# Kernel tuning notes

Hardware: AMD Instinct MI355X
Metric: run time of the kernel (lower is better)

## Reference

```python
import jax, jax.numpy as jnp
import numpy as np

N, E, T, S, R, L = 100000, 1600000, 4, 32, 16, 5
H = 3 * S  # out-head hidden (hidden_list=[n_scalars*3])
EPS = 1e-8


def _mlp(x, W1, b1, W2, b2):
    return jax.nn.silu(x @ W1 + b1) @ W2 + b2


def setup_inputs() -> dict:
    key = jax.random.key(0)
    ks = iter(jax.random.split(key, 40))
    rn = lambda *s: jax.random.normal(next(ks), s, dtype=jnp.float32)
    p = lambda *s: rn(*s) * 0.1
    inp = {
        'u': rn(N, T),
        'v': rn(N, T, 2),
        'boundary_norm': rn(N, 2),
        'is_boundary': jnp.zeros((N,), dtype=bool),
        'y_force': rn(N, 2),
        'pos': rn(N, 2),
        'edge_index': jax.random.randint(next(ks), (2, E), 0, N, dtype=jnp.int64),
        # node embedding MLP: invariant feats (2T+2) -> 2S -> S
        'Wn1': p(2 * T + 2, 2 * S), 'bn1': jnp.zeros((2 * S,)),
        'Wn2': p(2 * S, S), 'bn2': jnp.zeros((S,)),
        # L stacked InvBlock params: edge MLP (2S+R -> S -> S), node update (2S -> S -> S)
        'We1': p(L, 2 * S + R, S), 'be1': jnp.zeros((L, S)),
        'We2': p(L, S, S), 'be2': jnp.zeros((L, S)),
        'Wu1': p(L, 2 * S, S), 'bu1': jnp.zeros((L, S)),
        'Wu2': p(L, S, S), 'bu2': jnp.zeros((L, S)),
        'ln_g': jnp.ones((S,)), 'ln_b': jnp.zeros((S,)),
        # heads: S -> 3S -> {2,1}
        'Wr1': p(S, H), 'br1': jnp.zeros((H,)), 'Wr2': p(H, 2), 'br2': jnp.zeros((2,)),
        'Ws1': p(S, H), 'bs1': jnp.zeros((H,)), 'Ws2': p(H, 1), 'bs2': jnp.zeros((1,)),
    }
    return inp


def _forward(u, v, boundary_norm, y_force, pos, edge_index,
             Wn1, bn1, Wn2, bn2, We1, be1, We2, be2, Wu1, bu1, Wu2, bu2,
             ln_g, ln_b, Wr1, br1, Wr2, br2, Ws1, bs1, Ws2, bs2):
    # torch.no_grad() geometry branch: center positions, edge distances
    posc = jax.lax.stop_gradient(pos - pos.mean(axis=0))
    row, col = edge_index[0], edge_index[1]
    edge_vec = posc[row] - posc[col]                       # [E,2]
    dist = jnp.linalg.norm(edge_vec, axis=1)               # [E]
    # besel_linspace(start=0, end=1, number=R, cutoff=False): Bessel/sine RBF
    freqs = jnp.arange(1, R + 1, dtype=jnp.float32) * jnp.pi
    rbf = jnp.sqrt(2.0) * jnp.sin(dist[:, None] * freqs) / (dist[:, None] + EPS)  # [E,R]

    # Node_embedding_inv: SE(2)-invariant scalar features -> MLP
    feats = jnp.concatenate([
        u,                                                 # [N,T]
        jnp.linalg.norm(v, axis=-1),                       # [N,T]
        jnp.linalg.norm(boundary_norm, axis=-1, keepdims=True),
        jnp.linalg.norm(y_force, axis=-1, keepdims=True),
    ], axis=-1)                                            # [N,2T+2]
    x = _mlp(feats, Wn1, bn1, Wn2, bn2)                    # [N,S]

    # degree for mean aggregation (computed once)
    deg = jax.ops.segment_sum(jnp.ones((E,), jnp.float32), row, num_segments=N)
    inv_deg = 1.0 / jnp.maximum(deg, 1.0)                  # [N]

    for l in range(L):  # InvBlock message passing
        ef = jnp.concatenate([x[row], x[col], rbf], axis=-1)   # [E,2S+R]
        m = _mlp(ef, We1[l], be1[l], We2[l], be2[l])           # [E,S]
        agg = jax.ops.segment_sum(m, row, num_segments=N) * inv_deg[:, None]
        x = x + _mlp(jnp.concatenate([x, agg], axis=-1), Wu1[l], bu1[l], Wu2[l], bu2[l])

    # LayerNorm
    mu = x.mean(axis=-1, keepdims=True)
    var = jnp.var(x, axis=-1, keepdims=True)
    x = (x - mu) * jax.lax.rsqrt(var + 1e-5) * ln_g + ln_b

    v_ = _mlp(x, Wr1, br1, Wr2, br2)                       # [N,2]
    u_ = _mlp(x, Ws1, bs1, Ws2, bs2)                       # [N,1]
    return u[:, -1] + u_[:, 0], v_ + v[:, -1, :]


def reference(u, v, boundary_norm, is_boundary, y_force, pos, edge_index,
              Wn1, bn1, Wn2, bn2, We1, be1, We2, be2, Wu1, bu1, Wu2, bu2,
              ln_g, ln_b, Wr1, br1, Wr2, br2, Ws1, bs1, Ws2, bs2):
    del is_boundary  # unused by the visible forward
    return _forward(u, v, boundary_norm, y_force, pos, edge_index,
                    Wn1, bn1, Wn2, bn2, We1, be1, We2, be2, Wu1, bu1, Wu2, bu2,
                    ln_g, ln_b, Wr1, br1, Wr2, br2, Ws1, bs1, Ws2, bs2)
```

## Files before the change

### kernel.cpp

```cpp
#include <hip/hip_runtime.h>
#include <cmath>

namespace {

constexpr int N = 100000;
constexpr int E = 1600000;
constexpr int S = 32;
constexpr int L = 5;
constexpr int NB = (N + 255) / 256;
constexpr int NPW = 16;
constexpr int LB2 = (N + 63) / 64;
constexpr int NBKT = 391;
constexpr int EPB  = E / 256;
constexpr float PI_F    = 3.14159265358979323846f;
constexpr float SQRT2_F = 1.41421356237309515f;

typedef __attribute__((ext_vector_type(8))) short short8;
typedef __attribute__((ext_vector_type(4))) float f32x4;

__device__ __forceinline__ float silu_f(float x) {
    return x * __builtin_amdgcn_rcpf(1.0f + __expf(-x));
}

__device__ __forceinline__ unsigned short f2bf(float f) {
    unsigned int u = __float_as_uint(f);
    u = (u + 0x7FFFu + ((u >> 16) & 1u)) >> 16;
    return (unsigned short)u;
}

__device__ __forceinline__ int rl(int v, int i) {
    return __builtin_amdgcn_readlane(v, i);
}

__device__ __forceinline__ short8 ld_xb(const unsigned short* base, int col, int quad) {
    unsigned off = ((unsigned)col << 6) | ((unsigned)quad << 4);
    return *reinterpret_cast<const short8*>(reinterpret_cast<const char*>(base) + off);
}

__device__ __forceinline__ short8 ld_rbf(const unsigned short* base, int slot, int quad) {
    unsigned off = ((unsigned)slot << 5) | ((unsigned)quad << 4);
    return *reinterpret_cast<const short8*>(reinterpret_cast<const char*>(base) + off);
}

__device__ __forceinline__ void adv(int& i, int& t, int vd) {
    ++t;
    while (i < 16) {
        int dgi = rl(vd, i);
        int nt = (dgi + 15) >> 4;
        if (t < nt) break;
        t = 0; ++i;
    }
}

__device__ __forceinline__ int slotOf(int i, int t, int vs, int vd, int ml) {
    if (i >= 16) return 0;
    int s0 = rl(vs, i);
    int dg = rl(vd, i);
    int smax = s0 + ((dg > 0) ? dg : 1) - 1;
    int s = s0 + t * 16 + ml;
    return min(s, smax);
}

__global__ __launch_bounds__(256) void passA_kernel(
    const int* __restrict__ ei, int* __restrict__ hist)
{
    __shared__ int h[NBKT];
    int t = threadIdx.x;
    int blk = blockIdx.x;
    for (int b = t; b < NBKT; b += 256) h[b] = 0;
    __syncthreads();
    int base = blk * EPB;
    for (int i = t; i < EPB; i += 256) {
        int r = ei[base + i];
        atomicAdd(&h[r >> 8], 1);
    }
    __syncthreads();
    for (int b = t; b < NBKT; b += 256) hist[b * 256 + blk] = h[b];
}

__global__ __launch_bounds__(512) void p1_kernel(
    const int* __restrict__ hist, int* __restrict__ bstart)
{
    __shared__ int tot[NBKT + 1];
    int t = threadIdx.x;
    if (t < NBKT) {
        int s = 0;
        for (int b = 0; b < 256; ++b) s += hist[t * 256 + b];
        tot[t] = s;
    }
    __syncthreads();
    if (t == 0) {
        int a = 0;
        for (int i = 0; i < NBKT; ++i) { int c = tot[i]; tot[i] = a; a += c; }
        tot[NBKT] = a;
    }
    __syncthreads();
    if (t <= NBKT) bstart[t] = tot[t];
}

__global__ __launch_bounds__(256) void p2_kernel(
    const int* __restrict__ hist, const int* __restrict__ bstart,
    int* __restrict__ base)
{
    __shared__ int pre[256];
    int t = threadIdx.x;
    int bin = blockIdx.x;
    int h = hist[bin * 256 + t];
    pre[t] = h;
    __syncthreads();
    #pragma unroll
    for (int off = 1; off < 256; off <<= 1) {
        int v = (t >= off) ? pre[t - off] : 0;
        __syncthreads();
        pre[t] += v;
        __syncthreads();
    }
    base[bin * 256 + t] = bstart[bin] + pre[t] - h;
}

__global__ __launch_bounds__(256) void passB_kernel(
    const int* __restrict__ ei, const float* __restrict__ pos,
    const int* __restrict__ base, uint4* __restrict__ edgebuf)
{
    __shared__ int cur[NBKT];
    int t = threadIdx.x;
    int blk = blockIdx.x;
    for (int b = t; b < NBKT; b += 256) cur[b] = base[b * 256 + blk];
    __syncthreads();
    int ebase = blk * EPB;
    for (int i = t; i < EPB; i += 256) {
        int e = ebase + i;
        int r = ei[e];
        int c = ei[E + e];
        float2 pr = reinterpret_cast<const float2*>(pos)[r];
        float2 pc = reinterpret_cast<const float2*>(pos)[c];
        float dx = pr.x - pc.x, dy = pr.y - pc.y;
        float d = sqrtf(dx * dx + dy * dy);
        int slot = atomicAdd(&cur[r >> 8], 1);
        edgebuf[slot] = make_uint4((unsigned)c, __float_as_uint(d), (unsigned)r, 0u);
    }
}

__global__ __launch_bounds__(256) void passC_kernel(
    const uint4* __restrict__ edgebuf, const int* __restrict__ bstart,
    int* __restrict__ deg, int* __restrict__ start,
    int* __restrict__ csr_col, unsigned short* __restrict__ rbf_buf)
{
    __shared__ int cnt[256];
    __shared__ int pre[256];
    __shared__ int cur[256];
    int t = threadIdx.x;
    int bkt = blockIdx.x;
    int s0 = bstart[bkt], s1 = bstart[bkt + 1];

    cnt[t] = 0;
    __syncthreads();
    for (int i = s0 + t; i < s1; i += 256) {
        unsigned r = edgebuf[i].z;
        atomicAdd(&cnt[r & 255], 1);
    }
    __syncthreads();
    int c0 = cnt[t];
    pre[t] = c0;
    __syncthreads();
    #pragma unroll
    for (int off = 1; off < 256; off <<= 1) {
        int v = (t >= off) ? pre[t - off] : 0;
        __syncthreads();
        pre[t] += v;
        __syncthreads();
    }
    int row = bkt * 256 + t;
    int st = s0 + pre[t] - c0;
    if (row < N) {
        deg[row] = c0;
        start[row] = st;
    }
    cur[t] = st;
    __syncthreads();

    for (int i = s0 + t; i < s1; i += 256) {
        uint4 e = edgebuf[i];
        int slot = atomicAdd(&cur[e.z & 255], 1);
        csr_col[slot] = (int)e.x;
        float d = __uint_as_float(e.y);

        float sn = __sinf(PI_F * d);
        float c1 = __cosf(PI_F * d);
        float inv = SQRT2_F / (d + 1e-8f);
        float tc = 2.0f * c1;
        float sk = sn, skm = 0.0f;
        unsigned int pk[8];
        #pragma unroll
        for (int k = 0; k < 8; ++k) {
            float r0 = sk * inv;
            float s2 = tc * sk - skm; skm = sk; sk = s2;
            float r1 = sk * inv;
            float s3 = tc * sk - skm; skm = sk; sk = s3;
            pk[k] = (unsigned int)f2bf(r0) | ((unsigned int)f2bf(r1) << 16);
        }
        uint4* out = reinterpret_cast<uint4*>(rbf_buf + (size_t)slot * 16);
        out[0] = make_uint4(pk[0], pk[1], pk[2], pk[3]);
        out[1] = make_uint4(pk[4], pk[5], pk[6], pk[7]);
    }
}

__global__ __launch_bounds__(256) void prep_wt_kernel(
    const float* __restrict__ We1, const float* __restrict__ We2,
    const float* __restrict__ Wu1, const float* __restrict__ Wu2,
    short* __restrict__ wt1, short* __restrict__ wt2,
    short* __restrict__ wtu1, short* __restrict__ wtu2)
{
    int idx = blockIdx.x * 256 + threadIdx.x;
    if (idx < 5 * 32 * 96) {
        int l = idx / (32 * 96), r = idx % (32 * 96), n = r / 96, k = r % 96;
        float v = (k < 80) ? We1[((size_t)l * 80 + k) * 32 + n] : 0.0f;
        wt1[idx] = (short)f2bf(v);
    }
    if (idx < 5 * 32 * 32) {
        int l = idx / 1024, r = idx % 1024, n = r / 32, k = r % 32;
        wt2[idx]  = (short)f2bf(We2[((size_t)l * 32 + k) * 32 + n]);
        wtu2[idx] = (short)f2bf(Wu2[((size_t)l * 32 + k) * 32 + n]);
    }
    if (idx < 5 * 32 * 64) {
        int l = idx / 2048, r = idx % 2048, n = r / 64, k = r % 64;
        wtu1[idx] = (short)f2bf(Wu1[((size_t)l * 64 + k) * 32 + n]);
    }
}

__global__ __launch_bounds__(256) void node_embed_kernel(
    const float* __restrict__ u, const float* __restrict__ v,
    const float* __restrict__ bnorm, const float* __restrict__ yf,
    const float* __restrict__ Wn1, const float* __restrict__ bn1,
    const float* __restrict__ Wn2, const float* __restrict__ bn2,
    float* __restrict__ x, unsigned short* __restrict__ xb)
{
    int n = blockIdx.x * 256 + threadIdx.x;
    if (n >= N) return;

    float f[10];
    float4 uu = reinterpret_cast<const float4*>(u)[n];
    f[0] = uu.x; f[1] = uu.y; f[2] = uu.z; f[3] = uu.w;
    float4 v0 = reinterpret_cast<const float4*>(v)[2 * n];
    float4 v1 = reinterpret_cast<const float4*>(v)[2 * n + 1];
    f[4] = sqrtf(v0.x * v0.x + v0.y * v0.y);
    f[5] = sqrtf(v0.z * v0.z + v0.w * v0.w);
    f[6] = sqrtf(v1.x * v1.x + v1.y * v1.y);
    f[7] = sqrtf(v1.z * v1.z + v1.w * v1.w);
    float2 bb = reinterpret_cast<const float2*>(bnorm)[n];
    f[8] = sqrtf(bb.x * bb.x + bb.y * bb.y);
    float2 yy = reinterpret_cast<const float2*>(yf)[n];
    f[9] = sqrtf(yy.x * yy.x + yy.y * yy.y);

    float h[64];
    #pragma unroll
    for (int j = 0; j < 64; ++j) h[j] = bn1[j];
    #pragma unroll
    for (int i = 0; i < 10; ++i) {
        float t = f[i];
        #pragma unroll
        for (int j = 0; j < 64; ++j) h[j] = fmaf(t, Wn1[i * 64 + j], h[j]);
    }
    #pragma unroll
    for (int j = 0; j < 64; ++j) h[j] = silu_f(h[j]);

    float o[32];
    #pragma unroll
    for (int j = 0; j < 32; ++j) o[j] = bn2[j];
    #pragma unroll
    for (int i = 0; i < 64; ++i) {
        float t = h[i];
        #pragma unroll
        for (int j = 0; j < 32; ++j) o[j] = fmaf(t, Wn2[i * 32 + j], o[j]);
    }
    float4* xo = reinterpret_cast<float4*>(x + (size_t)n * 32);
    #pragma unroll
    for (int i = 0; i < 8; ++i)
        xo[i] = make_float4(o[4 * i], o[4 * i + 1], o[4 * i + 2], o[4 * i + 3]);

    unsigned int* xbu = reinterpret_cast<unsigned int*>(xb) + (size_t)n * 16;
    #pragma unroll
    for (int i = 0; i < 16; ++i)
        xbu[i] = (unsigned int)f2bf(o[2 * i]) | ((unsigned int)f2bf(o[2 * i + 1]) << 16);
}

__global__ __launch_bounds__(256, 4) void layer_kernel(
    const int* __restrict__ deg, const int* __restrict__ start,
    const int* __restrict__ csr_col, const unsigned short* __restrict__ rbf_buf,
    const float* __restrict__ x_in, const unsigned short* __restrict__ xb_in,
    float* __restrict__ x_out, unsigned short* __restrict__ xb_out,
    const short* __restrict__ wt1, const float* __restrict__ b1,
    const short* __restrict__ wt2, const float* __restrict__ b2,
    const short* __restrict__ wtu1, const float* __restrict__ bu1,
    const short* __restrict__ wtu2, const float* __restrict__ bu2)
{
    __shared__ unsigned short lsh[4][16 * 34];
    __shared__ unsigned short agb[4][16 * 34];
    __shared__ unsigned short hub[4][16 * 34];
    __shared__ float lx[4][16 * 33];
    __shared__ float lrp[4][16 * 33];
    __shared__ float ldg[4][16];
    __shared__ float livd[4][16];

    int t = threadIdx.x;
    int w = t >> 6;
    int lane = t & 63;
    int quad = lane >> 4;
    int ml = lane & 15;
    int wid = blockIdx.x * 4 + w;
    int nbase = __builtin_amdgcn_readfirstlane(wid * NPW);
    if (nbase >= N) return;

    int vs = start[nbase + ml];
    int vd = deg[nbase + ml];

    const short8* wp = reinterpret_cast<const short8*>(wt1);
    short8 B00 = wp[(ml     ) * 12 + 0 * 4 + quad];
    short8 B01 = wp[(ml     ) * 12 + 1 * 4 + quad];
    short8 B02 = wp[(ml     ) * 12 + 2 * 4 + quad];
    short8 B10 = wp[(ml + 16) * 12 + 0 * 4 + quad];
    short8 B11 = wp[(ml + 16) * 12 + 1 * 4 + quad];
    short8 B12 = wp[(ml + 16) * 12 + 2 * 4 + quad];

    short8 Ax = ld_xb(xb_in, nbase + ml, quad);

    float b1j0 = b1[ml];
    float b1j1 = b1[ml + 16];

    unsigned short* lshp = lsh[w];
    for (int k = lane; k < 16 * 34; k += 64) lshp[k] = 0;
    {
        const float* xs = x_in + (size_t)nbase * 32;
        float* lxp = lx[w];
        #pragma unroll
        for (int k = 0; k < 8; ++k) {
            int idx = lane * 8 + k;
            lxp[(idx >> 5) * 33 + (idx & 31)] = xs[idx];
        }
    }
    if (lane < 16) {
        ldg[w][lane] = (float)vd;
        livd[w][lane] = 1.0f / fmaxf((float)vd, 1.0f);
    }

    float* rpp = lrp[w];
    {
        f32x4 rp0 = {b1j0, b1j0, b1j0, b1j0};
        f32x4 rp1 = {b1j1, b1j1, b1j1, b1j1};
        rp0 = __builtin_amdgcn_mfma_f32_16x16x32_bf16(Ax, B00, rp0, 0, 0, 0);
        rp1 = __builtin_amdgcn_mfma_f32_16x16x32_bf16(Ax, B10, rp1, 0, 0, 0);
        int row = quad * 4;
        #pragma unroll
        for (int r = 0; r < 4; ++r) {
            rpp[(row + r) * 33 + ml]      = rp0[r];
            rpp[(row + r) * 33 + ml + 16] = rp1[r];
        }
    }
    __builtin_amdgcn_wave_barrier();

    const short8 Z8 = {0, 0, 0, 0, 0, 0, 0, 0};
    int i0 = 0, t0 = -1; adv(i0, t0, vd);
    int i1 = i0, t1 = t0; adv(i1, t1, vd);
    int i2 = i1, t2 = t1; adv(i2, t2, vd);

    int slot0 = slotOf(i0, t0, vs, vd, ml);
    int slot1 = slotOf(i1, t1, vs, vd, ml);
    int colCur  = csr_col[slot0];
    int colNext = csr_col[slot1];
    short8 A1c = ld_xb(xb_in, colCur, quad);
    short8 A2c = Z8;
    if (quad < 2) A2c = ld_rbf(rbf_buf, slot0, quad);

    float colp0 = 0.0f, colp1 = 0.0f;
    while (i0 < 16) {
        int slot2 = slotOf(i2, t2, vs, vd, ml);
        int colNN = csr_col[slot2];
        short8 A1n = ld_xb(xb_in, colNext, quad);
        short8 A2n = Z8;
        if (quad < 2) A2n = ld_rbf(rbf_buf, slot1, quad);

        float rpa = rpp[i0 * 33 + ml];
        float rpb = rpp[i0 * 33 + ml + 16];
        f32x4 acc0 = {rpa, rpa, rpa, rpa};
        f32x4 acc1 = {rpb, rpb, rpb, rpb};
        acc0 = __builtin_amdgcn_mfma_f32_16x16x32_bf16(A1c, B01, acc0, 0, 0, 0);
        acc0 = __builtin_amdgcn_mfma_f32_16x16x32_bf16(A2c, B02, acc0, 0, 0, 0);
        acc1 = __builtin_amdgcn_mfma_f32_16x16x32_bf16(A1c, B11, acc1, 0, 0, 0);
        acc1 = __builtin_amdgcn_mfma_f32_16x16x32_bf16(A2c, B12, acc1, 0, 0, 0);

        int dg0 = rl(vd, i0);
        int rowbase = t0 * 16 + quad * 4;
        #pragma unroll
        for (int r = 0; r < 4; ++r) {
            bool vld = (rowbase + r) < dg0;
            colp0 += vld ? silu_f(acc0[r]) : 0.0f;
            colp1 += vld ? silu_f(acc1[r]) : 0.0f;
        }
        if (t0 == ((dg0 + 15) >> 4) - 1) {
            colp0 += __shfl_xor(colp0, 16, 64);
            colp0 += __shfl_xor(colp0, 32, 64);
            colp1 += __shfl_xor(colp1, 16, 64);
            colp1 += __shfl_xor(colp1, 32, 64);
            if (quad == 0) {
                lshp[i0 * 34 + ml]      = f2bf(colp0);
                lshp[i0 * 34 + ml + 16] = f2bf(colp1);
            }
            colp0 = 0.0f; colp1 = 0.0f;
        }

        A1c = A1n; A2c = A2n;
        colNext = colNN; slot1 = slot2;
        i0 = i1; t0 = t1; i1 = i2; t1 = t2;
        adv(i2, t2, vd);
    }
    __builtin_amdgcn_wave_barrier();

    const short8* w2p = reinterpret_cast<const short8*>(wt2);
    short8 Bw2_0 = w2p[(ml     ) * 4 + quad];
    short8 Bw2_1 = w2p[(ml + 16) * 4 + quad];
    const short8* u1p = reinterpret_cast<const short8*>(wtu1);
    short8 Bu1_00 = u1p[(ml     ) * 8 + quad];
    short8 Bu1_10 = u1p[(ml     ) * 8 + 4 + quad];
    short8 Bu1_01 = u1p[(ml + 16) * 8 + quad];
    short8 Bu1_11 = u1p[(ml + 16) * 8 + 4 + quad];
    const short8* u2p = reinterpret_cast<const short8*>(wtu2);
    short8 Bu2_0 = u2p[(ml     ) * 4 + quad];
    short8 Bu2_1 = u2p[(ml + 16) * 4 + quad];

    short8 Ash = *reinterpret_cast<const short8*>(lshp + ml * 34 + quad * 8);
    f32x4 c0 = {0.0f, 0.0f, 0.0f, 0.0f};
    f32x4 c1 = {0.0f, 0.0f, 0.0f, 0.0f};
    c0 = __builtin_amdgcn_mfma_f32_16x16x32_bf16(Ash, Bw2_0, c0, 0, 0, 0);
    c1 = __builtin_amdgcn_mfma_f32_16x16x32_bf16(Ash, Bw2_1, c1, 0, 0, 0);
    float b2c0 = b2[ml], b2c1 = b2[ml + 16];
    unsigned short* agp = agb[w];
    int row = quad * 4;
    #pragma unroll
    for (int r = 0; r < 4; ++r) {
        float fd = ldg[w][row + r];
        float iv = livd[w][row + r];
        agp[(row + r) * 34 + ml]      = f2bf((c0[r] + fd * b2c0) * iv);
        agp[(row + r) * 34 + ml + 16] = f2bf((c1[r] + fd * b2c1) * iv);
    }
    __builtin_amdgcn_wave_barrier();

    short8 Aag = *reinterpret_cast<const short8*>(agp + ml * 34 + quad * 8);
    f32x4 d0 = {0.0f, 0.0f, 0.0f, 0.0f};
    f32x4 d1 = {0.0f, 0.0f, 0.0f, 0.0f};
    d0 = __builtin_amdgcn_mfma_f32_16x16x32_bf16(Ax,  Bu1_00, d0, 0, 0, 0);
    d0 = __builtin_amdgcn_mfma_f32_16x16x32_bf16(Aag, Bu1_10, d0, 0, 0, 0);
    d1 = __builtin_amdgcn_mfma_f32_16x16x32_bf16(Ax,  Bu1_01, d1, 0, 0, 0);
    d1 = __builtin_amdgcn_mfma_f32_16x16x32_bf16(Aag, Bu1_11, d1, 0, 0, 0);
    float bu1c0 = bu1[ml], bu1c1 = bu1[ml + 16];
    unsigned short* hup = hub[w];
    #pragma unroll
    for (int r = 0; r < 4; ++r) {
        hup[(row + r) * 34 + ml]      = f2bf(silu_f(d0[r] + bu1c0));
        hup[(row + r) * 34 + ml + 16] = f2bf(silu_f(d1[r] + bu1c1));
    }
    __builtin_amdgcn_wave_barrier();

    short8 Ahu = *reinterpret_cast<const short8*>(hup + ml * 34 + quad * 8);
    f32x4 e0 = {0.0f, 0.0f, 0.0f, 0.0f};
    f32x4 e1 = {0.0f, 0.0f, 0.0f, 0.0f};
    e0 = __builtin_amdgcn_mfma_f32_16x16x32_bf16(Ahu, Bu2_0, e0, 0, 0, 0);
    e1 = __builtin_amdgcn_mfma_f32_16x16x32_bf16(Ahu, Bu2_1, e1, 0, 0, 0);
    float bu2c0 = bu2[ml], bu2c1 = bu2[ml + 16];
    #pragma unroll
    for (int r = 0; r < 4; ++r) {
        int nn = nbase + row + r;
        float o0 = e0[r] + bu2c0 + lx[w][(row + r) * 33 + ml];
        float o1 = e1[r] + bu2c1 + lx[w][(row + r) * 33 + ml + 16];
        x_out[(size_t)nn * 32 + ml]      = o0;
        x_out[(size_t)nn * 32 + ml + 16] = o1;
        xb_out[(size_t)nn * 32 + ml]      = f2bf(o0);
        xb_out[(size_t)nn * 32 + ml + 16] = f2bf(o1);
    }
}

__global__ __launch_bounds__(256) void final_kernel(
    const float* __restrict__ x, const float* __restrict__ u,
    const float* __restrict__ v,
    const float* __restrict__ ln_g, const float* __restrict__ ln_b,
    const float* __restrict__ Wr1, const float* __restrict__ br1,
    const float* __restrict__ Wr2, const float* __restrict__ br2,
    const float* __restrict__ Ws1, const float* __restrict__ bs1,
    const float* __restrict__ Ws2, const float* __restrict__ bs2,
    float* __restrict__ out)
{
    int n = blockIdx.x * 256 + threadIdx.x;
    if (n >= N) return;

    float a[32];
    const float4* x4 = reinterpret_cast<const float4*>(x + (size_t)n * 32);
    #pragma unroll
    for (int i = 0; i < 8; ++i) {
        float4 t = x4[i];
        a[4 * i] = t.x; a[4 * i + 1] = t.y; a[4 * i + 2] = t.z; a[4 * i + 3] = t.w;
    }
    float mu = 0.0f;
    #pragma unroll
    for (int i = 0; i < 32; ++i) mu += a[i];
    mu *= (1.0f / 32.0f);
    float var = 0.0f;
    #pragma unroll
    for (int i = 0; i < 32; ++i) { float dlt = a[i] - mu; var += dlt * dlt; }
    var *= (1.0f / 32.0f);
    float rs = rsqrtf(var + 1e-5f);
    #pragma unroll
    for (int i = 0; i < 32; ++i) a[i] = (a[i] - mu) * rs * ln_g[i] + ln_b[i];

    float o0 = br2[0], o1 = br2[1], o2 = bs2[0];
    #pragma unroll 1
    for (int j = 0; j < 96; ++j) {
        float hr = br1[j];
        float hs = bs1[j];
        #pragma unroll
        for (int i = 0; i < 32; ++i) {
            hr = fmaf(a[i], Wr1[i * 96 + j], hr);
            hs = fmaf(a[i], Ws1[i * 96 + j], hs);
        }
        hr = silu_f(hr);
        hs = silu_f(hs);
        o0 = fmaf(hr, Wr2[2 * j], o0);
        o1 = fmaf(hr, Wr2[2 * j + 1], o1);
        o2 = fmaf(hs, Ws2[j], o2);
    }
    out[n] = u[n * 4 + 3] + o2;
    out[N + 2 * n]     = o0 + v[n * 8 + 6];
    out[N + 2 * n + 1] = o1 + v[n * 8 + 7];
}

}

extern "C" void kernel_launch(void* const* d_in, const int* in_sizes, int n_in,
                              void* d_out, int out_size, void* d_ws, size_t ws_size,
                              hipStream_t stream)
{
    const float* u    = (const float*)d_in[0];
    const float* v    = (const float*)d_in[1];
    const float* bno  = (const float*)d_in[2];
    const float* yf   = (const float*)d_in[4];
    const float* pos  = (const float*)d_in[5];
    const int*   ei   = (const int*)d_in[6];
    const float* Wn1  = (const float*)d_in[7];
    const float* bn1  = (const float*)d_in[8];
    const float* Wn2  = (const float*)d_in[9];
    const float* bn2  = (const float*)d_in[10];
    const float* We1  = (const float*)d_in[11];
    const float* be1  = (const float*)d_in[12];
    const float* We2  = (const float*)d_in[13];
    const float* be2  = (const float*)d_in[14];
    const float* Wu1  = (const float*)d_in[15];
    const float* bu1  = (const float*)d_in[16];
    const float* Wu2  = (const float*)d_in[17];
    const float* bu2  = (const float*)d_in[18];
    const float* ln_g = (const float*)d_in[19];
    const float* ln_b = (const float*)d_in[20];
    const float* Wr1  = (const float*)d_in[21];
    const float* br1  = (const float*)d_in[22];
    const float* Wr2  = (const float*)d_in[23];
    const float* br2  = (const float*)d_in[24];
    const float* Ws1  = (const float*)d_in[25];
    const float* bs1  = (const float*)d_in[26];
    const float* Ws2  = (const float*)d_in[27];
    const float* bs2  = (const float*)d_in[28];
    float* out = (float*)d_out;

    int*   deg      = (int*)d_ws;
    int*   start    = deg + N;
    int*   bstart   = start + N;
    int*   csr_col  = bstart + 512;
    unsigned short* rbf = (unsigned short*)(csr_col + E);
    float* x0       = (float*)(rbf + (size_t)E * 16);
    float* x1       = x0 + (size_t)N * S;
    unsigned short* xb0 = (unsigned short*)(x1 + (size_t)N * S);
    unsigned short* xb1 = xb0 + (size_t)N * S;
    short* wt1      = (short*)(xb1 + (size_t)N * S);
    short* wt2      = wt1 + 5 * 32 * 96;
    short* wtu1     = wt2 + 5 * 32 * 32;
    short* wtu2     = wtu1 + 5 * 32 * 64;
    int*   hist     = (int*)(wtu2 + 5 * 32 * 32);
    int*   basem    = hist + NBKT * 256;

    uint4* edgebuf = (uint4*)x0;

    passA_kernel<<<256, 256, 0, stream>>>(ei, hist);
    p1_kernel<<<1, 512, 0, stream>>>(hist, bstart);
    p2_kernel<<<NBKT, 256, 0, stream>>>(hist, bstart, basem);
    passB_kernel<<<256, 256, 0, stream>>>(ei, pos, basem, edgebuf);
    passC_kernel<<<NBKT, 256, 0, stream>>>(edgebuf, bstart, deg, start, csr_col, rbf);
    prep_wt_kernel<<<60, 256, 0, stream>>>(We1, We2, Wu1, Wu2, wt1, wt2, wtu1, wtu2);

    node_embed_kernel<<<NB, 256, 0, stream>>>(u, v, bno, yf, Wn1, bn1, Wn2, bn2,
                                              x0, xb0);

    float* xin = x0;  float* xout = x1;
    unsigned short* xbin = xb0;  unsigned short* xbout = xb1;
    for (int l = 0; l < L; ++l) {
        layer_kernel<<<LB2, 256, 0, stream>>>(
            deg, start, csr_col, rbf, xin, xbin, xout, xbout,
            wt1 + (size_t)l * 32 * 96,  be1 + (size_t)l * 32,
            wt2 + (size_t)l * 32 * 32,  be2 + (size_t)l * 32,
            wtu1 + (size_t)l * 32 * 64, bu1 + (size_t)l * 32,
            wtu2 + (size_t)l * 32 * 32, bu2 + (size_t)l * 32);
        float* tf = xin; xin = xout; xout = tf;
        unsigned short* tb = xbin; xbin = xbout; xbout = tb;
    }

    final_kernel<<<NB, 256, 0, stream>>>(xin, u, v, ln_g, ln_b,
                                         Wr1, br1, Wr2, br2,
                                         Ws1, bs1, Ws2, bs2, out);
}
```

Measured before the change: 572.6 us.

## Move output-head MLPs in final kernel onto bf16 MFMA

```diff
diff --git a/kernel.cpp b/kernel.cpp
--- a/kernel.cpp
+++ b/kernel.cpp
@@ -208,8 +208,10 @@
 __global__ __launch_bounds__(256) void prep_wt_kernel(
     const float* __restrict__ We1, const float* __restrict__ We2,
     const float* __restrict__ Wu1, const float* __restrict__ Wu2,
+    const float* __restrict__ Wr1, const float* __restrict__ Ws1,
     short* __restrict__ wt1, short* __restrict__ wt2,
-    short* __restrict__ wtu1, short* __restrict__ wtu2)
+    short* __restrict__ wtu1, short* __restrict__ wtu2,
+    short* __restrict__ wtr1, short* __restrict__ wts1)
 {
     int idx = blockIdx.x * 256 + threadIdx.x;
     if (idx < 5 * 32 * 96) {
@@ -225,6 +227,11 @@
     if (idx < 5 * 32 * 64) {
         int l = idx / 2048, r = idx % 2048, n = r / 64, k = r % 64;
         wtu1[idx] = (short)f2bf(Wu1[((size_t)l * 64 + k) * 32 + n]);
+    }
+    if (idx < 96 * 32) {
+        int n = idx / 32, k = idx % 32;
+        wtr1[idx] = (short)f2bf(Wr1[k * 96 + n]);
+        wts1[idx] = (short)f2bf(Ws1[k * 96 + n]);
     }
 }
 
@@ -482,53 +489,97 @@
     const float* __restrict__ x, const float* __restrict__ u,
     const float* __restrict__ v,
     const float* __restrict__ ln_g, const float* __restrict__ ln_b,
-    const float* __restrict__ Wr1, const float* __restrict__ br1,
+    const short* __restrict__ wtr1, const float* __restrict__ br1,
     const float* __restrict__ Wr2, const float* __restrict__ br2,
-    const float* __restrict__ Ws1, const float* __restrict__ bs1,
+    const short* __restrict__ wts1, const float* __restrict__ bs1,
     const float* __restrict__ Ws2, const float* __restrict__ bs2,
     float* __restrict__ out)
 {
-    int n = blockIdx.x * 256 + threadIdx.x;
-    if (n >= N) return;
-
-    float a[32];
-    const float4* x4 = reinterpret_cast<const float4*>(x + (size_t)n * 32);
-    #pragma unroll
-    for (int i = 0; i < 8; ++i) {
-        float4 t = x4[i];
-        a[4 * i] = t.x; a[4 * i + 1] = t.y; a[4 * i + 2] = t.z; a[4 * i + 3] = t.w;
-    }
-    float mu = 0.0f;
-    #pragma unroll
-    for (int i = 0; i < 32; ++i) mu += a[i];
-    mu *= (1.0f / 32.0f);
-    float var = 0.0f;
-    #pragma unroll
-    for (int i = 0; i < 32; ++i) { float dlt = a[i] - mu; var += dlt * dlt; }
-    var *= (1.0f / 32.0f);
+    int t = threadIdx.x;
+    int w = t >> 6;
+    int lane = t & 63;
+    int quad = lane >> 4;
+    int ml = lane & 15;
+    int wid = blockIdx.x * 4 + w;
+    int nbase = __builtin_amdgcn_readfirstlane(wid * NPW);
+    if (nbase >= N) return;
+
+    const float4* xs = reinterpret_cast<const float4*>(
+        x + (size_t)(nbase + ml) * 32 + quad * 8);
+    float4 xa = xs[0], xb4 = xs[1];
+    float f[8] = {xa.x, xa.y, xa.z, xa.w, xb4.x, xb4.y, xb4.z, xb4.w};
+
+    float s = 0.0f, ss = 0.0f;
+    #pragma unroll
+    for (int i = 0; i < 8; ++i) { s += f[i]; ss += f[i] * f[i]; }
+    s  += __shfl_xor(s, 16, 64);  s  += __shfl_xor(s, 32, 64);
+    ss += __shfl_xor(ss, 16, 64); ss += __shfl_xor(ss, 32, 64);
+    float mu = s * (1.0f / 32.0f);
+    float var = ss * (1.0f / 32.0f) - mu * mu;
     float rs = rsqrtf(var + 1e-5f);
-    #pragma unroll
-    for (int i = 0; i < 32; ++i) a[i] = (a[i] - mu) * rs * ln_g[i] + ln_b[i];
-
-    float o0 = br2[0], o1 = br2[1], o2 = bs2[0];
-    #pragma unroll 1
-    for (int j = 0; j < 96; ++j) {
-        float hr = br1[j];
-        float hs = bs1[j];
-        #pragma unroll
-        for (int i = 0; i < 32; ++i) {
-            hr = fmaf(a[i], Wr1[i * 96 + j], hr);
-            hs = fmaf(a[i], Ws1[i * 96 + j], hs);
+
+    const float4* gp = reinterpret_cast<const float4*>(ln_g + quad * 8);
+    const float4* bp = reinterpret_cast<const float4*>(ln_b + quad * 8);
+    float4 g0 = gp[0], g1 = gp[1], bb0 = bp[0], bb1 = bp[1];
+    float gg[8] = {g0.x, g0.y, g0.z, g0.w, g1.x, g1.y, g1.z, g1.w};
+    float bb[8] = {bb0.x, bb0.y, bb0.z, bb0.w, bb1.x, bb1.y, bb1.z, bb1.w};
+    short8 A;
+    #pragma unroll
+    for (int i = 0; i < 8; ++i)
+        A[i] = (short)f2bf((f[i] - mu) * rs * gg[i] + bb[i]);
+
+    const short8* r1p = reinterpret_cast<const short8*>(wtr1);
+    const short8* s1p = reinterpret_cast<const short8*>(wts1);
+    const f32x4 Zf = {0.0f, 0.0f, 0.0f, 0.0f};
+    f32x4 hr[6], hs[6];
+    #pragma unroll
+    for (int h = 0; h < 6; ++h) {
+        hr[h] = __builtin_amdgcn_mfma_f32_16x16x32_bf16(A, r1p[(ml + 16 * h) * 4 + quad], Zf, 0, 0, 0);
+        hs[h] = __builtin_amdgcn_mfma_f32_16x16x32_bf16(A, s1p[(ml + 16 * h) * 4 + quad], Zf, 0, 0, 0);
+    }
+
+    float wr2a[6], wr2b[6], ws2v[6], br1v[6], bs1v[6];
+    #pragma unroll
+    for (int h = 0; h < 6; ++h) {
+        int j = ml + 16 * h;
+        float2 wr = reinterpret_cast<const float2*>(Wr2)[j];
+        wr2a[h] = wr.x; wr2b[h] = wr.y;
+        ws2v[h] = Ws2[j];
+        br1v[h] = br1[j];
+        bs1v[h] = bs1[j];
+    }
+
+    float o0[4], o1[4], o2[4];
+    #pragma unroll
+    for (int r = 0; r < 4; ++r) {
+        float p0 = 0.0f, p1 = 0.0f, p2 = 0.0f;
+        #pragma unroll
+        for (int h = 0; h < 6; ++h) {
+            float a1 = silu_f(hr[h][r] + br1v[h]);
+            float a2 = silu_f(hs[h][r] + bs1v[h]);
+            p0 = fmaf(a1, wr2a[h], p0);
+            p1 = fmaf(a1, wr2b[h], p1);
+            p2 = fmaf(a2, ws2v[h], p2);
         }
-        hr = silu_f(hr);
-        hs = silu_f(hs);
-        o0 = fmaf(hr, Wr2[2 * j], o0);
-        o1 = fmaf(hr, Wr2[2 * j + 1], o1);
-        o2 = fmaf(hs, Ws2[j], o2);
-    }
-    out[n] = u[n * 4 + 3] + o2;
-    out[N + 2 * n]     = o0 + v[n * 8 + 6];
-    out[N + 2 * n + 1] = o1 + v[n * 8 + 7];
+        p0 += __shfl_xor(p0, 1, 64); p0 += __shfl_xor(p0, 2, 64);
+        p0 += __shfl_xor(p0, 4, 64); p0 += __shfl_xor(p0, 8, 64);
+        p1 += __shfl_xor(p1, 1, 64); p1 += __shfl_xor(p1, 2, 64);
+        p1 += __shfl_xor(p1, 4, 64); p1 += __shfl_xor(p1, 8, 64);
+        p2 += __shfl_xor(p2, 1, 64); p2 += __shfl_xor(p2, 2, 64);
+        p2 += __shfl_xor(p2, 4, 64); p2 += __shfl_xor(p2, 8, 64);
+        o0[r] = p0; o1[r] = p1; o2[r] = p2;
+    }
+
+    if (ml == 0) {
+        float b20 = br2[0], b21 = br2[1], b22 = bs2[0];
+        #pragma unroll
+        for (int r = 0; r < 4; ++r) {
+            int n = nbase + quad * 4 + r;
+            out[n] = u[n * 4 + 3] + o2[r] + b22;
+            out[N + 2 * n]     = o0[r] + b20 + v[n * 8 + 6];
+            out[N + 2 * n + 1] = o1[r] + b21 + v[n * 8 + 7];
+        }
+    }
 }
 
 }
@@ -580,7 +631,9 @@
     short* wt2      = wt1 + 5 * 32 * 96;
     short* wtu1     = wt2 + 5 * 32 * 32;
     short* wtu2     = wtu1 + 5 * 32 * 64;
-    int*   hist     = (int*)(wtu2 + 5 * 32 * 32);
+    short* wtr1     = wtu2 + 5 * 32 * 32;
+    short* wts1     = wtr1 + 96 * 32;
+    int*   hist     = (int*)(wts1 + 96 * 32);
     int*   basem    = hist + NBKT * 256;
 
     uint4* edgebuf = (uint4*)x0;
@@ -590,7 +643,8 @@
     p2_kernel<<<NBKT, 256, 0, stream>>>(hist, bstart, basem);
     passB_kernel<<<256, 256, 0, stream>>>(ei, pos, basem, edgebuf);
     passC_kernel<<<NBKT, 256, 0, stream>>>(edgebuf, bstart, deg, start, csr_col, rbf);
-    prep_wt_kernel<<<60, 256, 0, stream>>>(We1, We2, Wu1, Wu2, wt1, wt2, wtu1, wtu2);
+    prep_wt_kernel<<<60, 256, 0, stream>>>(We1, We2, Wu1, Wu2, Wr1, Ws1,
+                                           wt1, wt2, wtu1, wtu2, wtr1, wts1);
 
     node_embed_kernel<<<NB, 256, 0, stream>>>(u, v, bno, yf, Wn1, bn1, Wn2, bn2,
                                               x0, xb0);
@@ -608,7 +662,7 @@
         unsigned short* tb = xbin; xbin = xbout; xbout = tb;
     }
 
-    final_kernel<<<NB, 256, 0, stream>>>(xin, u, v, ln_g, ln_b,
-                                         Wr1, br1, Wr2, br2,
-                                         Ws1, bs1, Ws2, bs2, out);
-}
+    final_kernel<<<LB2, 256, 0, stream>>>(xin, u, v, ln_g, ln_b,
+                                          wtr1, br1, Wr2, br2,
+                                          wts1, bs1, Ws2, bs2, out);
+}
```

Result: faster. 526.3 us (-8.1%).
